# Performance work log

Hardware: AMD Instinct MI355X
Metric: run time of the kernel (lower is better)

## Reference

```python
import jax, jax.numpy as jnp
from jax import lax
import numpy as np

B, CIN, H, W = 8, 3, 512, 512
BASE = 32
TOPK = 200
SCORE_T = 0.01
IOU_T = 0.5
DN = ('NCHW', 'OIHW', 'NCHW')


def setup_inputs() -> dict:
    key = jax.random.key(0)
    ks = jax.random.split(key, 12)
    def conv_w(k, o, i, kh, kw):
        fan_in = i * kh * kw
        return jax.random.normal(k, (o, i, kh, kw), jnp.float32) * (1.0 / np.sqrt(fan_in))
    c = [CIN, BASE, BASE * 2, BASE * 4, BASE * 8]
    inp = {'images': jax.random.normal(ks[0], (B, CIN, H, W), jnp.float32)}
    for l in range(4):
        inp[f'w{l+1}'] = conv_w(ks[1 + 2 * l], c[l + 1], c[l], 3, 3)
        inp[f'b{l+1}'] = jnp.zeros((c[l + 1],), jnp.float32)
    inp['wh'] = conv_w(ks[9], 5, c[4], 1, 1)
    inp['bh'] = jnp.zeros((5,), jnp.float32)
    return inp


def _conv_relu_pool(x, w, b):
    x = lax.conv_general_dilated(x, w, (1, 1), 'SAME', dimension_numbers=DN)
    x = jax.nn.relu(x + b[None, :, None, None])
    return lax.reduce_window(x, -jnp.inf, lax.max, (1, 1, 2, 2), (1, 1, 2, 2), 'VALID')


def _decode(pred):
    # pred: [B,5,Gh,Gw]
    Bn, _, Gh, Gw = pred.shape
    sy, sx = H / float(Gh), W / float(Gw)
    obj = jax.nn.sigmoid(pred[:, 0])
    tx = jax.nn.sigmoid(pred[:, 1])
    ty = jax.nn.sigmoid(pred[:, 2])
    bw = jnp.exp(pred[:, 3]) * sx
    bh = jnp.exp(pred[:, 4]) * sy
    gy = jnp.arange(Gh, dtype=pred.dtype)[None, :, None]
    gx = jnp.arange(Gw, dtype=pred.dtype)[None, None, :]
    cx = gx * sx + tx * sx
    cy = gy * sy + ty * sy
    x1 = jnp.clip(cx - bw / 2.0, 0.0, W - 1)
    y1 = jnp.clip(cy - bh / 2.0, 0.0, H - 1)
    x2 = jnp.clip(cx + bw / 2.0, 0.0, W - 1)
    y2 = jnp.clip(cy + bh / 2.0, 0.0, H - 1)
    boxes = jnp.stack([x1, y1, x2, y2], axis=-1).reshape(Bn, Gh * Gw, 4)
    scores = obj.reshape(Bn, Gh * Gw)
    # score threshold + top-k (fixed size, padded with invalid entries)
    masked = jnp.where(scores >= SCORE_T, scores, -1.0)
    svals, sidx = lax.top_k(masked, TOPK)                      # [B,K]
    boxes_k = jnp.take_along_axis(boxes, sidx[:, :, None], axis=1)  # [B,K,4]
    valid = svals >= SCORE_T
    # pairwise IoU [B,K,K]
    bx1, by1, bx2, by2 = (boxes_k[..., i] for i in range(4))
    area = (bx2 - bx1) * (by2 - by1)
    xx1 = jnp.maximum(bx1[:, :, None], bx1[:, None, :])
    yy1 = jnp.maximum(by1[:, :, None], by1[:, None, :])
    xx2 = jnp.minimum(bx2[:, :, None], bx2[:, None, :])
    yy2 = jnp.minimum(by2[:, :, None], by2[:, None, :])
    inter = jnp.clip(xx2 - xx1, 0.0) * jnp.clip(yy2 - yy1, 0.0)
    union = area[:, :, None] + area[:, None, :] - inter
    iou = inter / jnp.maximum(union, 1e-6)
    ar = jnp.arange(TOPK)
    def body(i, keep):  # greedy NMS over score-sorted boxes
        sup = (iou[:, i, :] > IOU_T) & (ar[None, :] > i) & keep[:, i][:, None]
        return keep & ~sup
    keep = lax.fori_loop(0, TOPK, body, valid)
    scores_k = jnp.where(valid, svals, 0.0)
    return boxes_k, scores_k, keep


def reference(images, w1, b1, w2, b2, w3, b3, w4, b4, wh, bh):
    x = _conv_relu_pool(images, w1, b1)
    x = _conv_relu_pool(x, w2, b2)
    x = _conv_relu_pool(x, w3, b3)
    x = _conv_relu_pool(x, w4, b4)
    pred = lax.conv_general_dilated(x, wh, (1, 1), 'SAME', dimension_numbers=DN)
    pred = pred + bh[None, :, None, None]
    boxes, scores, keep = _decode(pred)
    kf = keep.astype(boxes.dtype)
    out5 = jnp.concatenate([boxes, scores[..., None]], axis=-1) * kf[..., None]
    return out5, keep
```

## Files before the change

kernel.cpp:

```cpp
#include <hip/hip_runtime.h>
#include <math.h>


constexpr int TOPK_N = 200;

template <int CIN, int CI_BLK, int CO_BLK>
__launch_bounds__(256)
__global__ void conv_relu_pool_pipe(const float* __restrict__ in,
                                    const float* __restrict__ wgt,
                                    const float* __restrict__ bias,
                                    float* __restrict__ out,
                                    int Hin, int Win, int Cout) {
    constexpr int SPATIAL = 34 * 34;
    constexpr int SSLOT = (SPATIAL + 255) / 256;
    constexpr int NW = CI_BLK * 9 * CO_BLK;
    constexpr int NCHUNK = CIN / CI_BLK;
    const int Hp = Hin >> 1, Wp = Win >> 1;
    const int coChunks = Cout / CO_BLK;
    const int b  = blockIdx.z / coChunks;
    const int cz = blockIdx.z % coChunks;
    const int tid = threadIdx.x;
    const int tx = tid & 15, ty = tid >> 4;
    const int px = (blockIdx.x << 4) + tx;
    const int py = (blockIdx.y << 4) + ty;
    const int iy0 = (blockIdx.y << 5) - 1;
    const int ix0 = (blockIdx.x << 5) - 1;

    __shared__ float  s_in[2][CI_BLK * SPATIAL];
    __shared__ double s_w[2][NW];

    int soff[SSLOT];
#pragma unroll
    for (int s = 0; s < SSLOT; ++s) {
        const int cell = tid + s * 256;
        int g = -1;
        if (cell < SPATIAL) {
            const int ly = cell / 34, lx = cell - ly * 34;
            const int iy = iy0 + ly, ix = ix0 + lx;
            if ((unsigned)iy < (unsigned)Hin && (unsigned)ix < (unsigned)Win)
                g = iy * Win + ix;
        }
        soff[s] = g;
    }
    int wg = -1;
    if (tid < NW) {
        const int co   = tid & (CO_BLK - 1);
        const int rest = tid / CO_BLK;
        const int k    = rest % 9;
        const int ci   = rest / 9;
        wg = ((cz * CO_BLK + co) * CIN + ci) * 9 + k;
    }
    const size_t HW = (size_t)Hin * Win;
    const float* in_b = in + (size_t)b * CIN * HW;

    double acc[CO_BLK][4];
#pragma unroll
    for (int co = 0; co < CO_BLK; ++co)
#pragma unroll
        for (int p = 0; p < 4; ++p) acc[co][p] = 0.0;

    float rin[CI_BLK][SSLOT];
    float rw = 0.f;

#pragma unroll
    for (int ci = 0; ci < CI_BLK; ++ci) {
        const float* src = in_b + ci * HW;
#pragma unroll
        for (int s = 0; s < SSLOT; ++s) {
            const int cell = tid + s * 256;
            float v = 0.f;
            if (cell < SPATIAL) { const int g = soff[s]; if (g >= 0) v = src[g]; }
            rin[ci][s] = v;
        }
    }
    if (tid < NW) rw = wgt[wg];
#pragma unroll
    for (int ci = 0; ci < CI_BLK; ++ci)
#pragma unroll
        for (int s = 0; s < SSLOT; ++s) {
            const int cell = tid + s * 256;
            if (cell < SPATIAL) s_in[0][ci * SPATIAL + cell] = rin[ci][s];
        }
    if (tid < NW) s_w[0][tid] = (double)rw;
    __syncthreads();

    for (int c = 0; c < NCHUNK; ++c) {
        const int buf = c & 1;
        if (c + 1 < NCHUNK) {
            const int c0n = (c + 1) * CI_BLK;
#pragma unroll
            for (int ci = 0; ci < CI_BLK; ++ci) {
                const float* src = in_b + (c0n + ci) * HW;
#pragma unroll
                for (int s = 0; s < SSLOT; ++s) {
                    const int cell = tid + s * 256;
                    float v = 0.f;
                    if (cell < SPATIAL) { const int g = soff[s]; if (g >= 0) v = src[g]; }
                    rin[ci][s] = v;
                }
            }
            if (tid < NW) rw = wgt[wg + c0n * 9];
        }
#pragma unroll 1
        for (int ci = 0; ci < CI_BLK; ++ci) {
            const float* tile = &s_in[buf][ci * SPATIAL];
            double win[4][4];
#pragma unroll
            for (int iy = 0; iy < 4; ++iy) {
                float2 r0 = *(const float2*)&tile[(2 * ty + iy) * 34 + 2 * tx];
                float2 r1 = *(const float2*)&tile[(2 * ty + iy) * 34 + 2 * tx + 2];
                win[iy][0] = (double)r0.x; win[iy][1] = (double)r0.y;
                win[iy][2] = (double)r1.x; win[iy][3] = (double)r1.y;
            }
#pragma unroll
            for (int k = 0; k < 9; ++k) {
                const int ky = k / 3, kx = k % 3;
                const double* wp = &s_w[buf][(ci * 9 + k) * CO_BLK];
                double w[CO_BLK];
#pragma unroll
                for (int co = 0; co < CO_BLK; ++co) w[co] = wp[co];
#pragma unroll
                for (int p = 0; p < 4; ++p) {
                    const double v = win[(p >> 1) + ky][(p & 1) + kx];
#pragma unroll
                    for (int co = 0; co < CO_BLK; ++co)
                        acc[co][p] = fma(v, w[co], acc[co][p]);
                }
            }
        }
        if (c + 1 < NCHUNK) {
#pragma unroll
            for (int ci = 0; ci < CI_BLK; ++ci)
#pragma unroll
                for (int s = 0; s < SSLOT; ++s) {
                    const int cell = tid + s * 256;
                    if (cell < SPATIAL) s_in[buf ^ 1][ci * SPATIAL + cell] = rin[ci][s];
                }
            if (tid < NW) s_w[buf ^ 1][tid] = (double)rw;
            __syncthreads();
        }
    }

#pragma unroll
    for (int co = 0; co < CO_BLK; ++co) {
        const double bd = (double)bias[cz * CO_BLK + co];
        const float e0 = fmaxf((float)(acc[co][0] + bd), 0.f);
        const float e1 = fmaxf((float)(acc[co][1] + bd), 0.f);
        const float e2 = fmaxf((float)(acc[co][2] + bd), 0.f);
        const float e3 = fmaxf((float)(acc[co][3] + bd), 0.f);
        out[((size_t)(b * Cout + cz * CO_BLK + co) * Hp + py) * Wp + px] =
            fmaxf(fmaxf(e0, e1), fmaxf(e2, e3));
    }
}

__launch_bounds__(256)
__global__ void head_decode_k(const float* __restrict__ x4,
                              const float* __restrict__ wh,
                              const float* __restrict__ bh,
                              float* __restrict__ boxes,
                              float* __restrict__ scores) {
    __shared__ float s_wh[5 * 256];
    const int tid = threadIdx.x;
#pragma unroll
    for (int i = 0; i < 5; ++i) s_wh[i * 256 + tid] = wh[i * 256 + tid];
    __syncthreads();

    const int idx  = blockIdx.x * 256 + tid;
    const int b    = idx >> 10;
    const int cell = idx & 1023;
    const int gy = cell >> 5, gx = cell & 31;

    double a0 = (double)bh[0], a1 = (double)bh[1], a2 = (double)bh[2],
           a3 = (double)bh[3], a4 = (double)bh[4];
    const float* xp = x4 + b * 262144 + cell;
    for (int ci = 0; ci < 256; ++ci) {
        const double v = (double)xp[ci << 10];
        a0 = fma(v, (double)s_wh[0 * 256 + ci], a0);
        a1 = fma(v, (double)s_wh[1 * 256 + ci], a1);
        a2 = fma(v, (double)s_wh[2 * 256 + ci], a2);
        a3 = fma(v, (double)s_wh[3 * 256 + ci], a3);
        a4 = fma(v, (double)s_wh[4 * 256 + ci], a4);
    }
    const double obj = 1.0 / (1.0 + exp(-a0));
    const double txs = 1.0 / (1.0 + exp(-a1));
    const double tys = 1.0 / (1.0 + exp(-a2));
    const double bw  = exp(a3) * 16.0;
    const double bhh = exp(a4) * 16.0;
    const double cx  = gx * 16.0 + txs * 16.0;
    const double cy  = gy * 16.0 + tys * 16.0;
    float* bp = boxes + idx * 4;
    bp[0] = (float)fmin(fmax(cx - bw * 0.5, 0.0), 511.0);
    bp[1] = (float)fmin(fmax(cy - bhh * 0.5, 0.0), 511.0);
    bp[2] = (float)fmin(fmax(cx + bw * 0.5, 0.0), 511.0);
    bp[3] = (float)fmin(fmax(cy + bhh * 0.5, 0.0), 511.0);
    scores[idx] = (float)obj;
}

__launch_bounds__(256)
__global__ void topk_nms_k(const float* __restrict__ boxes,
                           const float* __restrict__ scores,
                           float* __restrict__ out5,
                           float* __restrict__ keep_out) {
    const int b = blockIdx.x, tid = threadIdx.x;
    __shared__ unsigned long long key[1024];
    __shared__ float bx1[TOPK_N], by1[TOPK_N], bx2[TOPK_N], by2[TOPK_N];
    __shared__ float sv[TOPK_N], ar[TOPK_N];
    __shared__ int   kp[TOPK_N];

    for (int i = tid; i < 1024; i += 256) {
        float s = scores[b * 1024 + i];
        float m = (s >= 0.01f) ? s : -1.0f;
        unsigned u = __float_as_uint(m);
        u = (u & 0x80000000u) ? ~u : (u | 0x80000000u);
        key[i] = ((unsigned long long)u << 32) | (unsigned)(1023 - i);
    }
    __syncthreads();

    for (int k = 2; k <= 1024; k <<= 1) {
        for (int j = k >> 1; j > 0; j >>= 1) {
            for (int i = tid; i < 1024; i += 256) {
                int l = i ^ j;
                if (l > i) {
                    unsigned long long a = key[i], c = key[l];
                    bool desc = ((i & k) == 0);
                    bool sw = desc ? (a < c) : (a > c);
                    if (sw) { key[i] = c; key[l] = a; }
                }
            }
            __syncthreads();
        }
    }

    for (int i = tid; i < TOPK_N; i += 256) {
        unsigned long long kk = key[i];
        unsigned u = (unsigned)(kk >> 32);
        unsigned bits = (u & 0x80000000u) ? (u & 0x7FFFFFFFu) : ~u;
        float s = __uint_as_float(bits);
        int src = 1023 - (int)(kk & 0xFFFFFFFFu);
        const float4 bb = *(const float4*)(boxes + (b * 1024 + src) * 4);
        bx1[i] = bb.x; by1[i] = bb.y; bx2[i] = bb.z; by2[i] = bb.w;
        sv[i] = s;
        ar[i] = (bb.z - bb.x) * (bb.w - bb.y);
        kp[i] = (s >= 0.01f) ? 1 : 0;
    }
    __syncthreads();

    for (int i = 0; i < TOPK_N; ++i) {
        if (kp[i]) {
            const float X1 = bx1[i], Y1 = by1[i], X2 = bx2[i], Y2 = by2[i], A = ar[i];
            for (int j = tid; j < TOPK_N; j += 256) {
                if (j > i && kp[j]) {
                    float xx1 = fmaxf(X1, bx1[j]);
                    float yy1 = fmaxf(Y1, by1[j]);
                    float xx2 = fminf(X2, bx2[j]);
                    float yy2 = fminf(Y2, by2[j]);
                    float inter = fmaxf(xx2 - xx1, 0.f) * fmaxf(yy2 - yy1, 0.f);
                    float uni = A + ar[j] - inter;
                    float iou = inter / fmaxf(uni, 1e-6f);
                    if (iou > 0.5f) kp[j] = 0;
                }
            }
        }
        __syncthreads();
    }

    for (int i = tid; i < TOPK_N; i += 256) {
        float kf = kp[i] ? 1.f : 0.f;
        float s  = sv[i];
        float sc = (s >= 0.01f) ? s : 0.f;
        float* op = out5 + (b * TOPK_N + i) * 5;
        op[0] = bx1[i] * kf;
        op[1] = by1[i] * kf;
        op[2] = bx2[i] * kf;
        op[3] = by2[i] * kf;
        op[4] = sc * kf;
        keep_out[b * TOPK_N + i] = kf;
    }
}

extern "C" void kernel_launch(void* const* d_in, const int* in_sizes, int n_in,
                              void* d_out, int out_size, void* d_ws, size_t ws_size,
                              hipStream_t stream) {
    const float* images = (const float*)d_in[0];
    const float* w1 = (const float*)d_in[1];
    const float* b1 = (const float*)d_in[2];
    const float* w2 = (const float*)d_in[3];
    const float* b2 = (const float*)d_in[4];
    const float* w3 = (const float*)d_in[5];
    const float* b3 = (const float*)d_in[6];
    const float* w4 = (const float*)d_in[7];
    const float* b4 = (const float*)d_in[8];
    const float* wh = (const float*)d_in[9];
    const float* bh = (const float*)d_in[10];
    float* out = (float*)d_out;

    float* A    = (float*)d_ws;
    float* Bbuf = A + 16777216;
    float* boxes  = A + 8388608;
    float* scores = A + 8388608 + 32768;

    conv_relu_pool_pipe<3, 3, 8><<<dim3(16, 16, 8 * 4), 256, 0, stream>>>(
        images, w1, b1, A, 512, 512, 32);
    conv_relu_pool_pipe<32, 2, 8><<<dim3(8, 8, 8 * 8), 256, 0, stream>>>(
        A, w2, b2, Bbuf, 256, 256, 64);
    conv_relu_pool_pipe<64, 2, 8><<<dim3(4, 4, 8 * 16), 256, 0, stream>>>(
        Bbuf, w3, b3, A, 128, 128, 128);
    conv_relu_pool_pipe<128, 2, 8><<<dim3(2, 2, 8 * 32), 256, 0, stream>>>(
        A, w4, b4, Bbuf, 64, 64, 256);
    head_decode_k<<<32, 256, 0, stream>>>(Bbuf, wh, bh, boxes, scores);
    topk_nms_k<<<8, 256, 0, stream>>>(boxes, scores, out, out + 8 * TOPK_N * 5);
}
```

Before: 1.344 ms.

## Run conv layers 2-4 on FP64 MFMA implicit-GEMM kernel

Adds a new convolution kernel for layers 2-4 that treats the 3x3 conv as an implicit GEMM on the FP64 16x16x4 MFMA matrix instructions. Input tiles and weights are staged in double-buffered shared memory in 8-input-channel chunks, and ReLU plus 2x2 max-pool are fused into the epilogue using a cross-lane shuffle. The aim is to replace scalar double-precision FMA loops with matrix-core throughput while keeping FP64 accumulation for accuracy. The cost is more complex tiling and register pressure, and the grid is split differently.

```diff
diff --git a/kernel.cpp b/kernel.cpp
--- a/kernel.cpp
+++ b/kernel.cpp
@@ -3,6 +3,8 @@
 
 
 constexpr int TOPK_N = 200;
+
+typedef double f64x4 __attribute__((ext_vector_type(4)));
 
 template <int CIN, int CI_BLK, int CO_BLK>
 __launch_bounds__(256)
@@ -153,6 +155,175 @@
     }
 }
 
+template <int CIN>
+__launch_bounds__(256)
+__global__ void conv_mfma_f64(const float* __restrict__ in,
+                              const float* __restrict__ wgt,
+                              const float* __restrict__ bias,
+                              float* __restrict__ out,
+                              int Hin, int Win, int Cout) {
+    constexpr int TW = 34;
+    constexpr int CELLS = 34 * 10;
+    constexpr int CH = 360;
+    constexpr int CI_CHUNK = 8;
+    constexpr int NCHUNK = CIN / CI_CHUNK;
+    constexpr int WST = 296;
+
+    const int Hp = Hin >> 1, Wp = Win >> 1;
+    const int coChunks = Cout >> 5;
+    const int b   = blockIdx.z / coChunks;
+    const int cob = blockIdx.z % coChunks;
+    const int tid = threadIdx.x;
+    const int wv  = tid >> 6;
+    const int l15 = tid & 15;
+    const int l4  = (tid >> 4) & 3;
+    const int x0 = blockIdx.x << 5;
+    const int y0 = blockIdx.y << 3;
+
+    __shared__ float s_in[2][CI_CHUNK * CH];
+    __shared__ float s_w[2][CI_CHUNK * WST];
+
+    int soff[2];
+#pragma unroll
+    for (int s = 0; s < 2; ++s) {
+        const int cell = tid + s * 256;
+        int g = -1;
+        if (cell < CELLS) {
+            const int ly = cell / TW, lx = cell - ly * TW;
+            const int iy = y0 - 1 + ly, ix = x0 - 1 + lx;
+            if ((unsigned)iy < (unsigned)Hin && (unsigned)ix < (unsigned)Win)
+                g = iy * Win + ix;
+        }
+        soff[s] = g;
+    }
+    int wgoff[9], lwoff[9];
+#pragma unroll
+    for (int s = 0; s < 9; ++s) {
+        const int idx  = s * 256 + tid;
+        const int co_l = idx & 31;
+        const int r    = idx >> 5;
+        const int tap  = r % 9;
+        const int ci_l = r / 9;
+        wgoff[s] = ((cob * 32 + co_l) * CIN + ci_l) * 9 + tap;
+        lwoff[s] = ci_l * WST + tap * 32 + co_l;
+    }
+    const size_t HW = (size_t)Hin * Win;
+    const float* in_b = in + (size_t)b * CIN * HW;
+
+    int abase[4];
+#pragma unroll
+    for (int m = 0; m < 4; ++m) {
+        const int dy = m >> 1, xh = m & 1;
+        abase[m] = l4 * CH + (2 * wv + dy) * TW + xh * 16 + l15;
+    }
+    const int bbase0 = l4 * WST + l15;
+    const int bbase1 = l4 * WST + 16 + l15;
+
+    f64x4 acc[4][2];
+#pragma unroll
+    for (int m = 0; m < 4; ++m)
+#pragma unroll
+        for (int n = 0; n < 2; ++n)
+#pragma unroll
+            for (int j = 0; j < 4; ++j) acc[m][n][j] = 0.0;
+
+    float rin[CI_CHUNK][2];
+    float rwt[9];
+
+#pragma unroll
+    for (int ci = 0; ci < CI_CHUNK; ++ci) {
+        const float* src = in_b + (size_t)ci * HW;
+        rin[ci][0] = (soff[0] >= 0) ? src[soff[0]] : 0.f;
+        rin[ci][1] = (soff[1] >= 0) ? src[soff[1]] : 0.f;
+    }
+#pragma unroll
+    for (int s = 0; s < 9; ++s) rwt[s] = wgt[wgoff[s]];
+#pragma unroll
+    for (int ci = 0; ci < CI_CHUNK; ++ci) {
+        s_in[0][ci * CH + tid] = rin[ci][0];
+        if (tid < CELLS - 256) s_in[0][ci * CH + tid + 256] = rin[ci][1];
+    }
+#pragma unroll
+    for (int s = 0; s < 9; ++s) s_w[0][lwoff[s]] = rwt[s];
+    __syncthreads();
+
+#pragma unroll 2
+    for (int c = 0; c < NCHUNK; ++c) {
+        const int buf = c & 1;
+        if (c + 1 < NCHUNK) {
+            const int c0n = (c + 1) * CI_CHUNK;
+#pragma unroll
+            for (int ci = 0; ci < CI_CHUNK; ++ci) {
+                const float* src = in_b + (size_t)(c0n + ci) * HW;
+                rin[ci][0] = (soff[0] >= 0) ? src[soff[0]] : 0.f;
+                rin[ci][1] = (soff[1] >= 0) ? src[soff[1]] : 0.f;
+            }
+#pragma unroll
+            for (int s = 0; s < 9; ++s) rwt[s] = wgt[wgoff[s] + c0n * 9];
+        }
+        {
+            const float* ti = &s_in[buf][0];
+            const float* tw = &s_w[buf][0];
+#pragma unroll
+            for (int tap = 0; tap < 9; ++tap) {
+                const int ky = tap / 3, kx = tap % 3;
+#pragma unroll
+                for (int g = 0; g < 2; ++g) {
+                    const int ka = g * 4 * CH + ky * TW + kx;
+                    const int kb = g * 4 * WST + tap * 32;
+                    const double b0 = (double)tw[bbase0 + kb];
+                    const double b1 = (double)tw[bbase1 + kb];
+                    const double a0 = (double)ti[abase[0] + ka];
+                    const double a1 = (double)ti[abase[1] + ka];
+                    const double a2 = (double)ti[abase[2] + ka];
+                    const double a3 = (double)ti[abase[3] + ka];
+                    acc[0][0] = __builtin_amdgcn_mfma_f64_16x16x4f64(a0, b0, acc[0][0], 0, 0, 0);
+                    acc[0][1] = __builtin_amdgcn_mfma_f64_16x16x4f64(a0, b1, acc[0][1], 0, 0, 0);
+                    acc[1][0] = __builtin_amdgcn_mfma_f64_16x16x4f64(a1, b0, acc[1][0], 0, 0, 0);
+                    acc[1][1] = __builtin_amdgcn_mfma_f64_16x16x4f64(a1, b1, acc[1][1], 0, 0, 0);
+                    acc[2][0] = __builtin_amdgcn_mfma_f64_16x16x4f64(a2, b0, acc[2][0], 0, 0, 0);
+                    acc[2][1] = __builtin_amdgcn_mfma_f64_16x16x4f64(a2, b1, acc[2][1], 0, 0, 0);
+                    acc[3][0] = __builtin_amdgcn_mfma_f64_16x16x4f64(a3, b0, acc[3][0], 0, 0, 0);
+                    acc[3][1] = __builtin_amdgcn_mfma_f64_16x16x4f64(a3, b1, acc[3][1], 0, 0, 0);
+                }
+            }
+        }
+        if (c + 1 < NCHUNK) {
+#pragma unroll
+            for (int ci = 0; ci < CI_CHUNK; ++ci) {
+                s_in[buf ^ 1][ci * CH + tid] = rin[ci][0];
+                if (tid < CELLS - 256) s_in[buf ^ 1][ci * CH + tid + 256] = rin[ci][1];
+            }
+#pragma unroll
+            for (int s = 0; s < 9; ++s) s_w[buf ^ 1][lwoff[s]] = rwt[s];
+            __syncthreads();
+        }
+    }
+
+    const int yp = (y0 >> 1) + wv;
+#pragma unroll
+    for (int n = 0; n < 2; ++n) {
+        const int co = cob * 32 + n * 16 + l15;
+        const double bd = (double)bias[co];
+        float* orow = out + (((size_t)b * Cout + co) * Hp + yp) * Wp;
+#pragma unroll
+        for (int xh = 0; xh < 2; ++xh) {
+#pragma unroll
+            for (int r = 0; r < 4; ++r) {
+                const float e0 = fmaxf((float)(acc[xh][n][r]     + bd), 0.f);
+                const float e1 = fmaxf((float)(acc[2 + xh][n][r] + bd), 0.f);
+                float v = fmaxf(e0, e1);
+                const float p = __shfl_xor(v, 16, 64);
+                v = fmaxf(v, p);
+                if ((l4 & 1) == 0) {
+                    const int xp = (x0 >> 1) + xh * 8 + 2 * r + (l4 >> 1);
+                    orow[xp] = v;
+                }
+            }
+        }
+    }
+}
+
 __launch_bounds__(256)
 __global__ void head_decode_k(const float* __restrict__ x4,
                               const float* __restrict__ wh,
@@ -301,11 +472,11 @@
 
     conv_relu_pool_pipe<3, 3, 8><<<dim3(16, 16, 8 * 4), 256, 0, stream>>>(
         images, w1, b1, A, 512, 512, 32);
-    conv_relu_pool_pipe<32, 2, 8><<<dim3(8, 8, 8 * 8), 256, 0, stream>>>(
+    conv_mfma_f64<32><<<dim3(8, 32, 8 * 2), 256, 0, stream>>>(
         A, w2, b2, Bbuf, 256, 256, 64);
-    conv_relu_pool_pipe<64, 2, 8><<<dim3(4, 4, 8 * 16), 256, 0, stream>>>(
+    conv_mfma_f64<64><<<dim3(4, 16, 8 * 4), 256, 0, stream>>>(
         Bbuf, w3, b3, A, 128, 128, 128);
-    conv_relu_pool_pipe<128, 2, 8><<<dim3(2, 2, 8 * 32), 256, 0, stream>>>(
+    conv_mfma_f64<128><<<dim3(2, 8, 8 * 8), 256, 0, stream>>>(
         A, w4, b4, Bbuf, 64, 64, 256);
     head_decode_k<<<32, 256, 0, stream>>>(Bbuf, wh, bh, boxes, scores);
     topk_nms_k<<<8, 256, 0, stream>>>(boxes, scores, out, out + 8 * TOPK_N * 5);
```

New measurement: 1.386 ms. 1.03x slower.
